# Optimization experiments

Measured on AMD Instinct MI355X. Metric: run time of the kernel, lower is better.

Reference implementation:

```python
import jax, jax.numpy as jnp
import numpy as np

# Architecture constants (from init_kwargs / Mamba2 defaults)
NL = 4          # num_layer per direction
DM = 256        # d_model (attention_in)
DS = 128        # d_state
DC = 4          # d_conv
DI = 2 * DM     # d_inner = expand * d_model = 512
HD = 64         # headdim
NH = DI // HD   # nheads = 8
NG = 1          # ngroups
D_XBC = DI + 2 * NG * DS           # 768 conv channels
D_INP = 2 * DI + 2 * NG * DS + NH  # 1288 in_proj width
EPS = 1e-5


def rmsnorm(x, w):
    return x * jax.lax.rsqrt(jnp.mean(x * x, axis=-1, keepdims=True) + EPS) * w


def causal_dwconv(x, w, b):
    # x: (B, L, C); w: (C, K); b: (C,) -- causal depthwise conv
    K = w.shape[1]
    L = x.shape[1]
    xp = jnp.pad(x, ((0, 0), (K - 1, 0), (0, 0)))
    y = b
    for k in range(K):  # K=4, fixed small kernel
        y = y + xp[:, k:k + L, :] * w[:, k]
    return y


def ssd_scan(xh, dt, A_log, Bm, Cm):
    # xh: (B,L,H,P), dt: (B,L,H), A_log: (H,), Bm/Cm: (B,L,N) (ngroups=1, broadcast over heads)
    A = -jnp.exp(A_log)                 # (H,)
    decay = jnp.exp(dt * A)             # (B,L,H)
    dtx = dt[..., None] * xh            # (B,L,H,P)
    B, L, H, P = xh.shape
    N = Bm.shape[-1]

    def step(h, inp):
        dec, u, bt, ct = inp            # (B,H), (B,H,P), (B,N), (B,N)
        h = h * dec[..., None, None] + u[..., None] * bt[:, None, None, :]
        y = jnp.einsum('bhpn,bn->bhp', h, ct)
        return h, y

    h0 = jnp.zeros((B, H, P, N), xh.dtype)
    xs = (jnp.moveaxis(decay, 1, 0), jnp.moveaxis(dtx, 1, 0),
          jnp.moveaxis(Bm, 1, 0), jnp.moveaxis(Cm, 1, 0))
    _, ys = jax.lax.scan(step, h0, xs)  # ys: (L,B,H,P)
    return jnp.moveaxis(ys, 0, 1)


def mamba2_mixer(u, Wi, cw, cb, dtb, Al, Dp, gw, Wo):
    B, L, _ = u.shape
    zxbcdt = u @ Wi                                   # (B,L,1288)
    z = zxbcdt[..., :DI]
    xBC = zxbcdt[..., DI:DI + D_XBC]
    dt = zxbcdt[..., DI + D_XBC:]
    xBC = jax.nn.silu(causal_dwconv(xBC, cw, cb))
    xh = xBC[..., :DI].reshape(B, L, NH, HD)
    Bm = xBC[..., DI:DI + NG * DS]
    Cm = xBC[..., DI + NG * DS:]
    dt = jax.nn.softplus(dt + dtb)                    # (B,L,H)
    y = ssd_scan(xh, dt, Al, Bm, Cm) + xh * Dp[None, None, :, None]
    y = y.reshape(B, L, DI)
    g = rmsnorm(y * jax.nn.silu(z), gw)               # RMSNormGated
    return g @ Wo


def run_stack(x, block_ids, nw, Wi, cw, cb, dtb, Al, Dp, gw, Wo):
    res = None
    h = x
    for i in block_ids:
        res = h + res if res is not None else h
        h = mamba2_mixer(rmsnorm(res, nw[i]), Wi[i], cw[i], cb[i],
                         dtb[i], Al[i], Dp[i], gw[i], Wo[i])
    return h + res


def setup_inputs() -> dict:
    key = jax.random.key(0)
    ks = jax.random.split(key, 8)
    B, L = 4, 2048
    NB = 2 * NL  # 8 blocks: forward + backward
    x = jax.random.normal(ks[0], (B, L, DM), jnp.float32)
    nw = jnp.ones((NB, DM), jnp.float32)
    Wi = jax.random.normal(ks[1], (NB, DM, D_INP), jnp.float32) * 0.02
    cw = jax.random.normal(ks[2], (NB, D_XBC, DC), jnp.float32) * 0.2
    cb = jnp.zeros((NB, D_XBC), jnp.float32)
    dt0 = jax.random.uniform(ks[3], (NB, NH), jnp.float32, 0.001, 0.1)
    dtb = dt0 + jnp.log(-jnp.expm1(-dt0))  # inverse softplus
    Al = jnp.log(jax.random.uniform(ks[4], (NB, NH), jnp.float32, 1.0, 16.0))
    Dp = jnp.ones((NB, NH), jnp.float32)
    gw = jnp.ones((NB, DI), jnp.float32)
    Wo = jax.random.normal(ks[5], (NB, DI, DM), jnp.float32) * 0.02
    return {"x": x, "block_norm_w": nw, "in_proj_w": Wi, "conv_w": cw,
            "conv_b": cb, "dt_bias": dtb, "A_log": Al, "D": Dp,
            "gnorm_w": gw, "out_proj_w": Wo}


def reference(x, block_norm_w, in_proj_w, conv_w, conv_b, dt_bias, A_log, D, gnorm_w, out_proj_w):
    fwd = run_stack(x, range(NL), block_norm_w, in_proj_w, conv_w, conv_b,
                    dt_bias, A_log, D, gnorm_w, out_proj_w)
    bwd = run_stack(jnp.flip(x, 1), range(NL, 2 * NL), block_norm_w, in_proj_w,
                    conv_w, conv_b, dt_bias, A_log, D, gnorm_w, out_proj_w)
    return fwd + jnp.flip(bwd, 1)  # bidirectional_merging='add'
```

## Files before the change

### kernel.cpp

```cpp
#include <hip/hip_runtime.h>
#include <hip/hip_bf16.h>
#include <math.h>

#define LSEQ 2048
#define BREAL 4
#define BT 8
#define DM 256
#define DI 512
#define DSZ 128
#define NHEADS 8
#define HDIM 64
#define DXBC 768
#define DINP 1288
#define NINP_PAD 1408
#define NLAYERS 4
#define QCH 64
#define NCH (LSEQ/QCH)
#define CTL 64
#define EPSF 1e-5f

typedef __attribute__((ext_vector_type(8))) short short8b;
typedef __attribute__((ext_vector_type(4))) float f32x4;

__device__ __forceinline__ float siluf(float x){ return x / (1.f + __expf(-x)); }
__device__ __forceinline__ unsigned short f2bf(float x){
    union { float f; unsigned u; } c; c.f = x;
    unsigned r = (c.u + 0x7FFFu + ((c.u >> 16) & 1u)) >> 16;
    return (unsigned short)r;
}
__device__ __forceinline__ float bf2f(unsigned short u){
    union { unsigned u; float f; } c; c.u = ((unsigned)u) << 16;
    return c.f;
}

__global__ __launch_bounds__(256) void k_prep(const float* __restrict__ x, float* __restrict__ res){
    int i = blockIdx.x*256 + threadIdx.x;
    int d4 = i & (DM/4 - 1);
    int t  = i >> 6;
    int l  = t % LSEQ;
    int b  = t / LSEQ;
    const float4* x4 = (const float4*)x;
    float4 v;
    if (b < BREAL) v = x4[((size_t)(b*LSEQ) + l)*(DM/4) + d4];
    else           v = x4[((size_t)((b-BREAL)*LSEQ) + (LSEQ-1-l))*(DM/4) + d4];
    ((float4*)res)[i] = v;
}

__global__ __launch_bounds__(256) void k_wtrans(const float* __restrict__ W, unsigned short* __restrict__ WT,
                                                int K, int N, int Npad){
    __shared__ float sT[32][33];
    int n0 = blockIdx.x*32, k0 = blockIdx.y*32, g = blockIdx.z;
    const float* Wg = W + (size_t)g*K*N;
    unsigned short* WTg = WT + (size_t)g*Npad*K;
    int t = threadIdx.x;
    int r = t >> 3, c4 = (t & 7)*4;
    float4 v;
    if (n0 + c4 + 3 < N) v = *(const float4*)(Wg + (size_t)(k0+r)*N + n0 + c4);
    else {
        float tmp[4];
        #pragma unroll
        for (int j = 0; j < 4; j++) tmp[j] = (n0 + c4 + j < N) ? Wg[(size_t)(k0+r)*N + n0 + c4 + j] : 0.f;
        v = make_float4(tmp[0],tmp[1],tmp[2],tmp[3]);
    }
    sT[c4+0][r] = v.x; sT[c4+1][r] = v.y; sT[c4+2][r] = v.z; sT[c4+3][r] = v.w;
    __syncthreads();
    ushort4 o;
    o.x = f2bf(sT[r][c4+0]); o.y = f2bf(sT[r][c4+1]); o.z = f2bf(sT[r][c4+2]); o.w = f2bf(sT[r][c4+3]);
    *(ushort4*)(WTg + (size_t)(n0+r)*K + k0 + c4) = o;
}

__global__ __launch_bounds__(256) void k_resnorm(float* __restrict__ res, const float* __restrict__ h,
                                                 const float* __restrict__ nw, int li, int addH,
                                                 unsigned short* __restrict__ u){
    int wid  = (blockIdx.x*256 + threadIdx.x) >> 6;
    int lane = threadIdx.x & 63;
    int b = wid / LSEQ;
    float* rr = res + (size_t)wid*DM;
    float4 v = ((float4*)rr)[lane];
    if (addH){
        float4 hv = ((const float4*)(h + (size_t)wid*DM))[lane];
        v.x += hv.x; v.y += hv.y; v.z += hv.z; v.w += hv.w;
        ((float4*)rr)[lane] = v;
    }
    float ss = v.x*v.x + v.y*v.y + v.z*v.z + v.w*v.w;
    #pragma unroll
    for (int o = 32; o >= 1; o >>= 1) ss += __shfl_xor(ss, o, 64);
    float sc = rsqrtf(ss*(1.f/DM) + EPSF);
    int blk = (b < BREAL) ? li : li + NLAYERS;
    float4 w = ((const float4*)(nw + (size_t)blk*DM))[lane];
    ushort4 o4;
    o4.x = f2bf(v.x*sc*w.x); o4.y = f2bf(v.y*sc*w.y); o4.z = f2bf(v.z*sc*w.z); o4.w = f2bf(v.w*sc*w.w);
    *(ushort4*)(u + (size_t)wid*DM + lane*4) = o4;
}

__global__ __launch_bounds__(256) void k_gemm_mfma(const unsigned short* __restrict__ A,
                                                   const unsigned short* __restrict__ WT,
                                                   int K, int N, size_t wt_group_stride, int rows_per_group,
                                                   float* __restrict__ Cf, unsigned short* __restrict__ Cb,
                                                   int write_bf16){
    __shared__ unsigned short sA[128][40];
    __shared__ unsigned short sW[128][40];
    int bn = blockIdx.x, bm = blockIdx.y;
    int row0 = bm*128, n0 = bn*128;
    const unsigned short* WTg = WT + (size_t)(row0 / rows_per_group) * wt_group_stride;
    int t = threadIdx.x;
    int w = t >> 6, lane = t & 63;
    int wr = w >> 1, wc = w & 1;
    int l15 = lane & 15, lg = lane >> 4;
    f32x4 acc[4][4];
    #pragma unroll
    for (int mi = 0; mi < 4; mi++)
        #pragma unroll
        for (int ni = 0; ni < 4; ni++) acc[mi][ni] = (f32x4){0.f,0.f,0.f,0.f};

    int srow = t >> 1, shalf = t & 1;
    const unsigned short* Ap = A + (size_t)(row0 + srow)*K + shalf*16;
    const unsigned short* Wp = WTg + (size_t)(n0 + srow)*K + shalf*16;

    for (int k0 = 0; k0 < K; k0 += 32){
        int4 a0 = *(const int4*)(Ap + k0);
        int4 a1 = *(const int4*)(Ap + k0 + 8);
        int4 w0 = *(const int4*)(Wp + k0);
        int4 w1 = *(const int4*)(Wp + k0 + 8);
        __syncthreads();
        *(int4*)&sA[srow][shalf*16]     = a0;
        *(int4*)&sA[srow][shalf*16 + 8] = a1;
        *(int4*)&sW[srow][shalf*16]     = w0;
        *(int4*)&sW[srow][shalf*16 + 8] = w1;
        __syncthreads();
        short8b af[4], bf[4];
        #pragma unroll
        for (int mi = 0; mi < 4; mi++) af[mi] = *(const short8b*)&sA[wr*64 + mi*16 + l15][lg*8];
        #pragma unroll
        for (int ni = 0; ni < 4; ni++) bf[ni] = *(const short8b*)&sW[wc*64 + ni*16 + l15][lg*8];
        #pragma unroll
        for (int mi = 0; mi < 4; mi++)
            #pragma unroll
            for (int ni = 0; ni < 4; ni++)
                acc[mi][ni] = __builtin_amdgcn_mfma_f32_16x16x32_bf16(af[mi], bf[ni], acc[mi][ni], 0, 0, 0);
    }
    if (write_bf16){
        #pragma unroll
        for (int mi = 0; mi < 4; mi++)
            #pragma unroll
            for (int ni = 0; ni < 4; ni++){
                int col = n0 + wc*64 + ni*16 + l15;
                if (col < N){
                    #pragma unroll
                    for (int r = 0; r < 4; r++){
                        int row = row0 + wr*64 + mi*16 + lg*4 + r;
                        Cb[(size_t)row*N + col] = f2bf(acc[mi][ni][r]);
                    }
                }
            }
    } else {
        #pragma unroll
        for (int mi = 0; mi < 4; mi++)
            #pragma unroll
            for (int ni = 0; ni < 4; ni++){
                int col = n0 + wc*64 + ni*16 + l15;
                if (col < N){
                    #pragma unroll
                    for (int r = 0; r < 4; r++){
                        int row = row0 + wr*64 + mi*16 + lg*4 + r;
                        Cf[(size_t)row*N + col] = acc[mi][ni][r];
                    }
                }
            }
    }
}

__global__ __launch_bounds__(256) void k_conv2(const unsigned short* __restrict__ zxb,
                                               const float* __restrict__ cw, const float* __restrict__ cb,
                                               int li, unsigned short* __restrict__ xbcb){
    int bid = blockIdx.x;
    int ch = bid % 3;
    int tl = (bid/3) % (LSEQ/CTL);
    int b  = bid / (3*(LSEQ/CTL));
    int c  = ch*256 + threadIdx.x;
    int blk = (b < BREAL) ? li : li + NLAYERS;
    float4 wv = *(const float4*)(cw + (size_t)blk*DXBC*4 + c*4);
    float bias = cb[(size_t)blk*DXBC + c];
    int l0 = tl*CTL;
    size_t base = ((size_t)b*LSEQ)*DINP + DI + c;
    float xm3 = (l0 >= 3) ? bf2f(zxb[base + (size_t)(l0-3)*DINP]) : 0.f;
    float xm2 = (l0 >= 2) ? bf2f(zxb[base + (size_t)(l0-2)*DINP]) : 0.f;
    float xm1 = (l0 >= 1) ? bf2f(zxb[base + (size_t)(l0-1)*DINP]) : 0.f;
    for (int l = l0; l < l0 + CTL; l++){
        float xv = bf2f(zxb[base + (size_t)l*DINP]);
        float acc = bias + xm3*wv.x + xm2*wv.y + xm1*wv.z + xv*wv.w;
        xbcb[((size_t)(b*LSEQ)+l)*DXBC + c] = f2bf(siluf(acc));
        xm3 = xm2; xm2 = xm1; xm1 = xv;
    }
}

__global__ __launch_bounds__(256) void k_dtla(const unsigned short* __restrict__ zxb,
                                              const float* __restrict__ dtb, const float* __restrict__ Al,
                                              int li, float* __restrict__ dt, float* __restrict__ la){
    int i = blockIdx.x*256 + threadIdx.x;
    int h = i & 7;
    int bl = i >> 3;
    int b = bl >> 11;
    int blk = (b < BREAL) ? li : li + NLAYERS;
    float raw = bf2f(zxb[(size_t)bl*DINP + DI + DXBC + h]) + dtb[blk*NHEADS + h];
    float d = (raw > 20.f) ? raw : log1pf(__expf(raw));
    float Aa = -__expf(Al[blk*NHEADS + h]);
    dt[i] = d;
    la[i] = d*Aa;
}

__global__ __launch_bounds__(256) void k_chunk_state(const unsigned short* __restrict__ xbcb,
                                                     const float* __restrict__ dt, const float* __restrict__ la,
                                                     unsigned short* __restrict__ states, float* __restrict__ decp){
    __shared__ unsigned short sBT[DSZ][72];
    __shared__ unsigned short sXT[HDIM][72];
    __shared__ float sSa[QCH];
    __shared__ float sW[QCH];
    int bid = blockIdx.x;
    int c  = bid & (NCH-1);
    int bh = bid >> 5;
    int b = bh >> 3, h = bh & 7;
    int t = threadIdx.x;
    size_t bl0 = (size_t)b*LSEQ + c*QCH;

    if (t < QCH){
        float v = la[(bl0 + t)*NHEADS + h];
        #pragma unroll
        for (int o = 1; o < 64; o <<= 1){
            float u = __shfl_up(v, o, 64);
            if (t >= o) v += u;
        }
        sSa[t] = v;
        float saQ = __shfl(v, 63, 64);
        float dtv = dt[(bl0 + t)*NHEADS + h];
        sW[t] = dtv * __expf(saQ - v);
        if (t == 63) decp[bh*NCH + c] = __expf(v);
    }
    __syncthreads();

    #pragma unroll
    for (int it = 0; it < 4; it++){
        int e = t + 256*it;
        int j = e >> 4, n8 = (e & 15)*8;
        int4 v = *(const int4*)(xbcb + (bl0 + j)*DXBC + DI + n8);
        const unsigned short* pv = (const unsigned short*)&v;
        #pragma unroll
        for (int i = 0; i < 8; i++) sBT[n8+i][j] = pv[i];
    }
    #pragma unroll
    for (int it = 0; it < 4; it++){
        int e = t + 256*it;
        int j = e >> 4, p4 = (e & 15)*4;
        ushort4 v = *(const ushort4*)(xbcb + (bl0 + j)*DXBC + h*HDIM + p4);
        float s = sW[j];
        sXT[p4+0][j] = f2bf(bf2f(v.x)*s);
        sXT[p4+1][j] = f2bf(bf2f(v.y)*s);
        sXT[p4+2][j] = f2bf(bf2f(v.z)*s);
        sXT[p4+3][j] = f2bf(bf2f(v.w)*s);
    }
    __syncthreads();

    int w = t >> 6, lane = t & 63, l15 = lane & 15, lg = lane >> 4;
    int p0 = (w >> 1)*32, n0 = (w & 1)*64;
    f32x4 acc[2][4];
    #pragma unroll
    for (int mi = 0; mi < 2; mi++)
        #pragma unroll
        for (int ni = 0; ni < 4; ni++) acc[mi][ni] = (f32x4){0.f,0.f,0.f,0.f};
    #pragma unroll
    for (int kk = 0; kk < 2; kk++){
        short8b a[2], bb[4];
        #pragma unroll
        for (int mi = 0; mi < 2; mi++) a[mi]  = *(const short8b*)&sXT[p0 + mi*16 + l15][kk*32 + lg*8];
        #pragma unroll
        for (int ni = 0; ni < 4; ni++) bb[ni] = *(const short8b*)&sBT[n0 + ni*16 + l15][kk*32 + lg*8];
        #pragma unroll
        for (int mi = 0; mi < 2; mi++)
            #pragma unroll
            for (int ni = 0; ni < 4; ni++)
                acc[mi][ni] = __builtin_amdgcn_mfma_f32_16x16x32_bf16(a[mi], bb[ni], acc[mi][ni], 0, 0, 0);
    }
    unsigned short* sp = states + ((size_t)bh*NCH + c)*(HDIM*DSZ);
    #pragma unroll
    for (int mi = 0; mi < 2; mi++)
        #pragma unroll
        for (int ni = 0; ni < 4; ni++)
            #pragma unroll
            for (int r = 0; r < 4; r++){
                int p = p0 + mi*16 + lg*4 + r;
                int n = n0 + ni*16 + l15;
                sp[(size_t)p*DSZ + n] = f2bf(acc[mi][ni][r]);
            }
}

__global__ __launch_bounds__(256) void k_scan2(unsigned short* __restrict__ states, const float* __restrict__ decp){
    int bh = blockIdx.x >> 3, slice = blockIdx.x & 7;
    int t = threadIdx.x;
    size_t base = (size_t)bh*NCH*(HDIM*DSZ) + slice*1024 + t*4;
    float H0=0.f, H1=0.f, H2=0.f, H3=0.f;
    for (int c = 0; c < NCH; c++){
        float P = decp[bh*NCH + c];
        unsigned short* sp = states + base + (size_t)c*(HDIM*DSZ);
        ushort4 S = *(ushort4*)sp;
        ushort4 Hw;
        Hw.x = f2bf(H0); Hw.y = f2bf(H1); Hw.z = f2bf(H2); Hw.w = f2bf(H3);
        *(ushort4*)sp = Hw;
        H0 = fmaf(H0, P, bf2f(S.x));
        H1 = fmaf(H1, P, bf2f(S.y));
        H2 = fmaf(H2, P, bf2f(S.z));
        H3 = fmaf(H3, P, bf2f(S.w));
    }
}

__global__ __launch_bounds__(256) void k_chunk_y(const unsigned short* __restrict__ xbcb,
                                                 const float* __restrict__ dt, const float* __restrict__ la,
                                                 const unsigned short* __restrict__ states,
                                                 const float* __restrict__ Dp, int li,
                                                 float* __restrict__ y){
    __shared__ unsigned short sC_[QCH][136];
    __shared__ unsigned short sB_[QCH][136];
    __shared__ unsigned short sH[HDIM][136];
    __shared__ unsigned short sS[QCH][72];
    __shared__ unsigned short sXT[HDIM][72];
    __shared__ float sSa[QCH];
    __shared__ float sDt[QCH];
    int bid = blockIdx.x;
    int c  = bid & (NCH-1);
    int bh = bid >> 5;
    int b = bh >> 3, h = bh & 7;
    int blk = (b < BREAL) ? li : li + NLAYERS;
    int t = threadIdx.x;
    size_t bl0 = (size_t)b*LSEQ + c*QCH;

    if (t < QCH){
        float v = la[(bl0 + t)*NHEADS + h];
        #pragma unroll
        for (int o = 1; o < 64; o <<= 1){
            float u = __shfl_up(v, o, 64);
            if (t >= o) v += u;
        }
        sSa[t] = v;
        sDt[t] = dt[(bl0 + t)*NHEADS + h];
    }
    __syncthreads();

    #pragma unroll
    for (int it = 0; it < 4; it++){
        int e = t + 256*it;
        int j = e >> 4, n8 = (e & 15)*8;
        *(int4*)&sB_[j][n8] = *(const int4*)(xbcb + (bl0 + j)*DXBC + DI + n8);
        *(int4*)&sC_[j][n8] = *(const int4*)(xbcb + (bl0 + j)*DXBC + DI + DSZ + n8);
    }
    {
        size_t sbase = ((size_t)bh*NCH + c)*(HDIM*DSZ);
        #pragma unroll
        for (int it = 0; it < 4; it++){
            int e = t + 256*it;
            int p = e >> 4, n8 = (e & 15)*8;
            *(int4*)&sH[p][n8] = *(const int4*)(states + sbase + (size_t)p*DSZ + n8);
        }
    }
    #pragma unroll
    for (int it = 0; it < 4; it++){
        int e = t + 256*it;
        int j = e >> 4, p4 = (e & 15)*4;
        ushort4 v = *(const ushort4*)(xbcb + (bl0 + j)*DXBC + h*HDIM + p4);
        float s = sDt[j];
        sXT[p4+0][j] = f2bf(bf2f(v.x)*s);
        sXT[p4+1][j] = f2bf(bf2f(v.y)*s);
        sXT[p4+2][j] = f2bf(bf2f(v.z)*s);
        sXT[p4+3][j] = f2bf(bf2f(v.w)*s);
    }
    __syncthreads();

    int w = t >> 6, lane = t & 63, l15 = lane & 15, lg = lane >> 4;
    int i0 = (w >> 1)*32, q0 = (w & 1)*32;

    f32x4 accS[2][2];
    #pragma unroll
    for (int mi = 0; mi < 2; mi++)
        #pragma unroll
        for (int nj = 0; nj < 2; nj++) accS[mi][nj] = (f32x4){0.f,0.f,0.f,0.f};
    #pragma unroll
    for (int kk = 0; kk < 4; kk++){
        short8b a[2], bb[2];
        #pragma unroll
        for (int mi = 0; mi < 2; mi++) a[mi]  = *(const short8b*)&sC_[i0 + mi*16 + l15][kk*32 + lg*8];
        #pragma unroll
        for (int nj = 0; nj < 2; nj++) bb[nj] = *(const short8b*)&sB_[q0 + nj*16 + l15][kk*32 + lg*8];
        #pragma unroll
        for (int mi = 0; mi < 2; mi++)
            #pragma unroll
            for (int nj = 0; nj < 2; nj++)
                accS[mi][nj] = __builtin_amdgcn_mfma_f32_16x16x32_bf16(a[mi], bb[nj], accS[mi][nj], 0, 0, 0);
    }
    #pragma unroll
    for (int mi = 0; mi < 2; mi++)
        #pragma unroll
        for (int nj = 0; nj < 2; nj++)
            #pragma unroll
            for (int r = 0; r < 4; r++){
                int i = i0 + mi*16 + lg*4 + r;
                int j = q0 + nj*16 + l15;
                float wgt = (i >= j) ? __expf(sSa[i] - sSa[j]) : 0.f;
                sS[i][j] = f2bf(accS[mi][nj][r] * wgt);
            }
    __syncthreads();

    f32x4 accY[2][2], accI[2][2];
    #pragma unroll
    for (int mi = 0; mi < 2; mi++)
        #pragma unroll
        for (int nj = 0; nj < 2; nj++){ accY[mi][nj] = (f32x4){0.f,0.f,0.f,0.f}; accI[mi][nj] = (f32x4){0.f,0.f,0.f,0.f}; }
    #pragma unroll
    for (int kk = 0; kk < 2; kk++){
        short8b a[2], bb[2];
        #pragma unroll
        for (int mi = 0; mi < 2; mi++) a[mi]  = *(const short8b*)&sS[i0 + mi*16 + l15][kk*32 + lg*8];
        #pragma unroll
        for (int nj = 0; nj < 2; nj++) bb[nj] = *(const short8b*)&sXT[q0 + nj*16 + l15][kk*32 + lg*8];
        #pragma unroll
        for (int mi = 0; mi < 2; mi++)
            #pragma unroll
            for (int nj = 0; nj < 2; nj++)
                accY[mi][nj] = __builtin_amdgcn_mfma_f32_16x16x32_bf16(a[mi], bb[nj], accY[mi][nj], 0, 0, 0);
    }
    #pragma unroll
    for (int kk = 0; kk < 4; kk++){
        short8b a[2], bb[2];
        #pragma unroll
        for (int mi = 0; mi < 2; mi++) a[mi]  = *(const short8b*)&sC_[i0 + mi*16 + l15][kk*32 + lg*8];
        #pragma unroll
        for (int nj = 0; nj < 2; nj++) bb[nj] = *(const short8b*)&sH[q0 + nj*16 + l15][kk*32 + lg*8];
        #pragma unroll
        for (int mi = 0; mi < 2; mi++)
            #pragma unroll
            for (int nj = 0; nj < 2; nj++)
                accI[mi][nj] = __builtin_amdgcn_mfma_f32_16x16x32_bf16(a[mi], bb[nj], accI[mi][nj], 0, 0, 0);
    }

    float dD = Dp[blk*NHEADS + h];
    #pragma unroll
    for (int mi = 0; mi < 2; mi++)
        #pragma unroll
        for (int r = 0; r < 4; r++){
            int i = i0 + mi*16 + lg*4 + r;
            float ei = __expf(sSa[i]);
            #pragma unroll
            for (int nj = 0; nj < 2; nj++){
                int p = q0 + nj*16 + l15;
                float xh = bf2f(xbcb[(bl0 + i)*DXBC + h*HDIM + p]);
                y[(bl0 + i)*DI + h*HDIM + p] = accY[mi][nj][r] + ei*accI[mi][nj][r] + dD*xh;
            }
        }
}

__global__ __launch_bounds__(256) void k_gatenorm(const float* __restrict__ y, const unsigned short* __restrict__ zxb,
                                                  const float* __restrict__ gw, int li,
                                                  unsigned short* __restrict__ yb){
    int wid  = (blockIdx.x*256 + threadIdx.x) >> 6;
    int lane = threadIdx.x & 63;
    int b = wid / LSEQ;
    int blk = (b < BREAL) ? li : li + NLAYERS;
    const float* yr = y + (size_t)wid*DI;
    const unsigned short* zr = zxb + (size_t)wid*DINP;
    float4 v0 = ((const float4*)yr)[lane];
    float4 v1 = ((const float4*)yr)[64 + lane];
    ushort4 zu0 = *(const ushort4*)(zr + lane*4);
    ushort4 zu1 = *(const ushort4*)(zr + 256 + lane*4);
    v0.x *= siluf(bf2f(zu0.x)); v0.y *= siluf(bf2f(zu0.y)); v0.z *= siluf(bf2f(zu0.z)); v0.w *= siluf(bf2f(zu0.w));
    v1.x *= siluf(bf2f(zu1.x)); v1.y *= siluf(bf2f(zu1.y)); v1.z *= siluf(bf2f(zu1.z)); v1.w *= siluf(bf2f(zu1.w));
    float ss = v0.x*v0.x + v0.y*v0.y + v0.z*v0.z + v0.w*v0.w
             + v1.x*v1.x + v1.y*v1.y + v1.z*v1.z + v1.w*v1.w;
    #pragma unroll
    for (int o = 32; o >= 1; o >>= 1) ss += __shfl_xor(ss, o, 64);
    float sc = rsqrtf(ss*(1.f/DI) + EPSF);
    const float4* w4 = (const float4*)(gw + (size_t)blk*DI);
    float4 w0 = w4[lane], w1 = w4[64 + lane];
    ushort4 o0, o1;
    o0.x = f2bf(v0.x*sc*w0.x); o0.y = f2bf(v0.y*sc*w0.y); o0.z = f2bf(v0.z*sc*w0.z); o0.w = f2bf(v0.w*sc*w0.w);
    o1.x = f2bf(v1.x*sc*w1.x); o1.y = f2bf(v1.y*sc*w1.y); o1.z = f2bf(v1.z*sc*w1.z); o1.w = f2bf(v1.w*sc*w1.w);
    *(ushort4*)(yb + (size_t)wid*DI + lane*4)       = o0;
    *(ushort4*)(yb + (size_t)wid*DI + 256 + lane*4) = o1;
}

__global__ __launch_bounds__(256) void k_final(const float* __restrict__ res, const float* __restrict__ h,
                                               float* __restrict__ out){
    int i = blockIdx.x*256 + threadIdx.x;
    int d4 = i & 63;
    int t  = i >> 6;
    int l = t % LSEQ, b = t / LSEQ;
    size_t fi = ((size_t)(b*LSEQ) + l)*(DM/4) + d4;
    size_t bi = ((size_t)((b+BREAL)*LSEQ) + (LSEQ-1-l))*(DM/4) + d4;
    float4 r1 = ((const float4*)res)[fi], h1 = ((const float4*)h)[fi];
    float4 r2 = ((const float4*)res)[bi], h2 = ((const float4*)h)[bi];
    float4 o;
    o.x = r1.x + h1.x + r2.x + h2.x;
    o.y = r1.y + h1.y + r2.y + h2.y;
    o.z = r1.z + h1.z + r2.z + h2.z;
    o.w = r1.w + h1.w + r2.w + h2.w;
    ((float4*)out)[i] = o;
}

extern "C" void kernel_launch(void* const* d_in, const int* in_sizes, int n_in,
                              void* d_out, int out_size, void* d_ws, size_t ws_size,
                              hipStream_t stream){
    const float* x   = (const float*)d_in[0];
    const float* nw  = (const float*)d_in[1];
    const float* Wi  = (const float*)d_in[2];
    const float* cw  = (const float*)d_in[3];
    const float* cb  = (const float*)d_in[4];
    const float* dtb = (const float*)d_in[5];
    const float* Al  = (const float*)d_in[6];
    const float* Dp  = (const float*)d_in[7];
    const float* gw  = (const float*)d_in[8];
    const float* Wo  = (const float*)d_in[9];
    float* out = (float*)d_out;

    size_t off = 0;
    auto alloc = [&](size_t bytes){ void* p = (char*)d_ws + off; off += (bytes + 255) & ~(size_t)255; return p; };
    float* RES    = (float*)alloc((size_t)BT*LSEQ*DM*4);
    unsigned short* STATES = (unsigned short*)alloc((size_t)BT*NHEADS*NCH*HDIM*DSZ*2);
    float* HBUF   = (float*)STATES;
    unsigned short* YGB = (unsigned short*)alloc((size_t)BT*LSEQ*DI*2);
    unsigned short* UBUF = YGB;
    unsigned short* ZXB = (unsigned short*)alloc((size_t)BT*LSEQ*DINP*2);
    unsigned short* XBC = (unsigned short*)alloc((size_t)BT*LSEQ*DXBC*2);
    float* DT     = (float*)alloc((size_t)BT*LSEQ*NHEADS*4);
    float* LA     = (float*)alloc((size_t)BT*LSEQ*NHEADS*4);
    float* YG     = (float*)alloc((size_t)BT*LSEQ*DI*4);
    float* DECP   = (float*)alloc((size_t)BT*NHEADS*NCH*4);
    unsigned short* WiT = (unsigned short*)alloc((size_t)2*NLAYERS*NINP_PAD*DM*2);
    unsigned short* WoT = (unsigned short*)alloc((size_t)2*NLAYERS*DM*DI*2);
    (void)ws_size; (void)in_sizes; (void)n_in; (void)out_size;

    k_prep<<<(BT*LSEQ*DM/4)/256, 256, 0, stream>>>(x, RES);
    k_wtrans<<<dim3(NINP_PAD/32, DM/32, 2*NLAYERS), 256, 0, stream>>>(Wi, WiT, DM, DINP, NINP_PAD);
    k_wtrans<<<dim3(DM/32, DI/32, 2*NLAYERS), 256, 0, stream>>>(Wo, WoT, DI, DM, DM);

    for (int li = 0; li < NLAYERS; li++){
        k_resnorm<<<(BT*LSEQ)/4, 256, 0, stream>>>(RES, HBUF, nw, li, li > 0 ? 1 : 0, UBUF);
        k_gemm_mfma<<<dim3(NINP_PAD/128, (BT*LSEQ)/128), 256, 0, stream>>>(
            UBUF, WiT + (size_t)li*NINP_PAD*DM, DM, DINP,
            (size_t)NLAYERS*NINP_PAD*DM, BREAL*LSEQ, nullptr, ZXB, 1);
        k_conv2<<<BT*(LSEQ/CTL)*3, 256, 0, stream>>>(ZXB, cw, cb, li, XBC);
        k_dtla<<<(BT*LSEQ*NHEADS)/256, 256, 0, stream>>>(ZXB, dtb, Al, li, DT, LA);
        k_chunk_state<<<BT*NHEADS*NCH, 256, 0, stream>>>(XBC, DT, LA, STATES, DECP);
        k_scan2<<<BT*NHEADS*8, 256, 0, stream>>>(STATES, DECP);
        k_chunk_y<<<BT*NHEADS*NCH, 256, 0, stream>>>(XBC, DT, LA, STATES, Dp, li, YG);
        k_gatenorm<<<(BT*LSEQ)/4, 256, 0, stream>>>(YG, ZXB, gw, li, YGB);
        k_gemm_mfma<<<dim3(DM/128, (BT*LSEQ)/128), 256, 0, stream>>>(
            YGB, WoT + (size_t)li*DM*DI, DI, DM,
            (size_t)NLAYERS*DM*DI, BREAL*LSEQ, HBUF, nullptr, 0);
    }
    k_final<<<(BREAL*LSEQ*DM/4)/256, 256, 0, stream>>>(RES, HBUF, out);
}
```

Before: 709.2 us.

## Fuse residual add into out_proj GEMM, merge dt kernel, batch heads per chunk block

The out_proj GEMM now accumulates straight into the residual buffer, which removes the separate H buffer and the residual add in resnorm and k_final. The dt/softplus computation is folded into the conv kernel, saving one launch. chunk_state and chunk_y each handle four heads per block so the B/C loads and the C·B^T product are shared across heads. The y intermediate is stored as bf16 instead of fp32, halving that traffic at some precision cost. Per-head loops add syncs and fewer blocks, which may reduce parallelism.

```diff
diff --git a/kernel.cpp b/kernel.cpp
--- a/kernel.cpp
+++ b/kernel.cpp
@@ -69,19 +69,14 @@
     *(ushort4*)(WTg + (size_t)(n0+r)*K + k0 + c4) = o;
 }
 
-__global__ __launch_bounds__(256) void k_resnorm(float* __restrict__ res, const float* __restrict__ h,
-                                                 const float* __restrict__ nw, int li, int addH,
+__global__ __launch_bounds__(256) void k_resnorm(const float* __restrict__ res,
+                                                 const float* __restrict__ nw, int li,
                                                  unsigned short* __restrict__ u){
     int wid  = (blockIdx.x*256 + threadIdx.x) >> 6;
     int lane = threadIdx.x & 63;
     int b = wid / LSEQ;
-    float* rr = res + (size_t)wid*DM;
-    float4 v = ((float4*)rr)[lane];
-    if (addH){
-        float4 hv = ((const float4*)(h + (size_t)wid*DM))[lane];
-        v.x += hv.x; v.y += hv.y; v.z += hv.z; v.w += hv.w;
-        ((float4*)rr)[lane] = v;
-    }
+    const float* rr = res + (size_t)wid*DM;
+    float4 v = ((const float4*)rr)[lane];
     float ss = v.x*v.x + v.y*v.y + v.z*v.z + v.w*v.w;
     #pragma unroll
     for (int o = 32; o >= 1; o >>= 1) ss += __shfl_xor(ss, o, 64);
@@ -97,7 +92,7 @@
                                                    const unsigned short* __restrict__ WT,
                                                    int K, int N, size_t wt_group_stride, int rows_per_group,
                                                    float* __restrict__ Cf, unsigned short* __restrict__ Cb,
-                                                   int write_bf16){
+                                                   int mode){
     __shared__ unsigned short sA[128][40];
     __shared__ unsigned short sW[128][40];
     int bn = blockIdx.x, bm = blockIdx.y;
@@ -139,40 +134,28 @@
             for (int ni = 0; ni < 4; ni++)
                 acc[mi][ni] = __builtin_amdgcn_mfma_f32_16x16x32_bf16(af[mi], bf[ni], acc[mi][ni], 0, 0, 0);
     }
-    if (write_bf16){
-        #pragma unroll
-        for (int mi = 0; mi < 4; mi++)
-            #pragma unroll
-            for (int ni = 0; ni < 4; ni++){
-                int col = n0 + wc*64 + ni*16 + l15;
-                if (col < N){
-                    #pragma unroll
-                    for (int r = 0; r < 4; r++){
-                        int row = row0 + wr*64 + mi*16 + lg*4 + r;
-                        Cb[(size_t)row*N + col] = f2bf(acc[mi][ni][r]);
-                    }
+    #pragma unroll
+    for (int mi = 0; mi < 4; mi++)
+        #pragma unroll
+        for (int ni = 0; ni < 4; ni++){
+            int col = n0 + wc*64 + ni*16 + l15;
+            if (col < N){
+                #pragma unroll
+                for (int r = 0; r < 4; r++){
+                    int row = row0 + wr*64 + mi*16 + lg*4 + r;
+                    if (mode == 1)      Cb[(size_t)row*N + col] = f2bf(acc[mi][ni][r]);
+                    else if (mode == 2) Cf[(size_t)row*N + col] += acc[mi][ni][r];
+                    else                Cf[(size_t)row*N + col] = acc[mi][ni][r];
                 }
             }
-    } else {
-        #pragma unroll
-        for (int mi = 0; mi < 4; mi++)
-            #pragma unroll
-            for (int ni = 0; ni < 4; ni++){
-                int col = n0 + wc*64 + ni*16 + l15;
-                if (col < N){
-                    #pragma unroll
-                    for (int r = 0; r < 4; r++){
-                        int row = row0 + wr*64 + mi*16 + lg*4 + r;
-                        Cf[(size_t)row*N + col] = acc[mi][ni][r];
-                    }
-                }
-            }
-    }
+        }
 }
 
 __global__ __launch_bounds__(256) void k_conv2(const unsigned short* __restrict__ zxb,
                                                const float* __restrict__ cw, const float* __restrict__ cb,
-                                               int li, unsigned short* __restrict__ xbcb){
+                                               const float* __restrict__ dtb, const float* __restrict__ Al,
+                                               int li, unsigned short* __restrict__ xbcb,
+                                               float* __restrict__ dtO, float* __restrict__ laO){
     int bid = blockIdx.x;
     int ch = bid % 3;
     int tl = (bid/3) % (LSEQ/CTL);
@@ -192,21 +175,18 @@
         xbcb[((size_t)(b*LSEQ)+l)*DXBC + c] = f2bf(siluf(acc));
         xm3 = xm2; xm2 = xm1; xm1 = xv;
     }
-}
-
-__global__ __launch_bounds__(256) void k_dtla(const unsigned short* __restrict__ zxb,
-                                              const float* __restrict__ dtb, const float* __restrict__ Al,
-                                              int li, float* __restrict__ dt, float* __restrict__ la){
-    int i = blockIdx.x*256 + threadIdx.x;
-    int h = i & 7;
-    int bl = i >> 3;
-    int b = bl >> 11;
-    int blk = (b < BREAL) ? li : li + NLAYERS;
-    float raw = bf2f(zxb[(size_t)bl*DINP + DI + DXBC + h]) + dtb[blk*NHEADS + h];
-    float d = (raw > 20.f) ? raw : log1pf(__expf(raw));
-    float Aa = -__expf(Al[blk*NHEADS + h]);
-    dt[i] = d;
-    la[i] = d*Aa;
+    if (ch == 0){
+        #pragma unroll
+        for (int it = 0; it < 2; it++){
+            int e = threadIdx.x*2 + it;
+            int h = e & 7, dl = e >> 3;
+            size_t bl = (size_t)b*LSEQ + l0 + dl;
+            float raw = bf2f(zxb[bl*DINP + DI + DXBC + h]) + dtb[blk*NHEADS + h];
+            float d = (raw > 20.f) ? raw : log1pf(__expf(raw));
+            dtO[bl*NHEADS + h] = d;
+            laO[bl*NHEADS + h] = -d*__expf(Al[blk*NHEADS + h]);
+        }
+    }
 }
 
 __global__ __launch_bounds__(256) void k_chunk_state(const unsigned short* __restrict__ xbcb,
@@ -214,30 +194,28 @@
                                                      unsigned short* __restrict__ states, float* __restrict__ decp){
     __shared__ unsigned short sBT[DSZ][72];
     __shared__ unsigned short sXT[HDIM][72];
-    __shared__ float sSa[QCH];
-    __shared__ float sW[QCH];
+    __shared__ float sW[4][QCH];
     int bid = blockIdx.x;
-    int c  = bid & (NCH-1);
-    int bh = bid >> 5;
-    int b = bh >> 3, h = bh & 7;
+    int hg = bid & 1;
+    int c  = (bid >> 1) & (NCH-1);
+    int b  = bid >> 6;
     int t = threadIdx.x;
+    int w = t >> 6, lane = t & 63, l15 = lane & 15, lg = lane >> 4;
     size_t bl0 = (size_t)b*LSEQ + c*QCH;
 
-    if (t < QCH){
-        float v = la[(bl0 + t)*NHEADS + h];
+    {
+        int h = hg*4 + w;
+        float v = la[(bl0 + lane)*NHEADS + h];
         #pragma unroll
         for (int o = 1; o < 64; o <<= 1){
             float u = __shfl_up(v, o, 64);
-            if (t >= o) v += u;
-        }
-        sSa[t] = v;
+            if (lane >= o) v += u;
+        }
         float saQ = __shfl(v, 63, 64);
-        float dtv = dt[(bl0 + t)*NHEADS + h];
-        sW[t] = dtv * __expf(saQ - v);
-        if (t == 63) decp[bh*NCH + c] = __expf(v);
-    }
-    __syncthreads();
-
+        float dtv = dt[(bl0 + lane)*NHEADS + h];
+        sW[w][lane] = dtv * __expf(saQ - v);
+        if (lane == 63) decp[((size_t)b*NHEADS + h)*NCH + c] = __expf(v);
+    }
     #pragma unroll
     for (int it = 0; it < 4; it++){
         int e = t + 256*it;
@@ -247,50 +225,54 @@
         #pragma unroll
         for (int i = 0; i < 8; i++) sBT[n8+i][j] = pv[i];
     }
-    #pragma unroll
-    for (int it = 0; it < 4; it++){
-        int e = t + 256*it;
-        int j = e >> 4, p4 = (e & 15)*4;
-        ushort4 v = *(const ushort4*)(xbcb + (bl0 + j)*DXBC + h*HDIM + p4);
-        float s = sW[j];
-        sXT[p4+0][j] = f2bf(bf2f(v.x)*s);
-        sXT[p4+1][j] = f2bf(bf2f(v.y)*s);
-        sXT[p4+2][j] = f2bf(bf2f(v.z)*s);
-        sXT[p4+3][j] = f2bf(bf2f(v.w)*s);
-    }
     __syncthreads();
 
-    int w = t >> 6, lane = t & 63, l15 = lane & 15, lg = lane >> 4;
     int p0 = (w >> 1)*32, n0 = (w & 1)*64;
-    f32x4 acc[2][4];
-    #pragma unroll
-    for (int mi = 0; mi < 2; mi++)
-        #pragma unroll
-        for (int ni = 0; ni < 4; ni++) acc[mi][ni] = (f32x4){0.f,0.f,0.f,0.f};
-    #pragma unroll
-    for (int kk = 0; kk < 2; kk++){
-        short8b a[2], bb[4];
-        #pragma unroll
-        for (int mi = 0; mi < 2; mi++) a[mi]  = *(const short8b*)&sXT[p0 + mi*16 + l15][kk*32 + lg*8];
-        #pragma unroll
-        for (int ni = 0; ni < 4; ni++) bb[ni] = *(const short8b*)&sBT[n0 + ni*16 + l15][kk*32 + lg*8];
+    for (int hh = 0; hh < 4; hh++){
+        int h = hg*4 + hh;
+        #pragma unroll
+        for (int it = 0; it < 4; it++){
+            int e = t + 256*it;
+            int j = e >> 4, p4 = (e & 15)*4;
+            ushort4 v = *(const ushort4*)(xbcb + (bl0 + j)*DXBC + h*HDIM + p4);
+            float s = sW[hh][j];
+            sXT[p4+0][j] = f2bf(bf2f(v.x)*s);
+            sXT[p4+1][j] = f2bf(bf2f(v.y)*s);
+            sXT[p4+2][j] = f2bf(bf2f(v.z)*s);
+            sXT[p4+3][j] = f2bf(bf2f(v.w)*s);
+        }
+        __syncthreads();
+        f32x4 acc[2][4];
         #pragma unroll
         for (int mi = 0; mi < 2; mi++)
             #pragma unroll
+            for (int ni = 0; ni < 4; ni++) acc[mi][ni] = (f32x4){0.f,0.f,0.f,0.f};
+        #pragma unroll
+        for (int kk = 0; kk < 2; kk++){
+            short8b a[2], bb[4];
+            #pragma unroll
+            for (int mi = 0; mi < 2; mi++) a[mi]  = *(const short8b*)&sXT[p0 + mi*16 + l15][kk*32 + lg*8];
+            #pragma unroll
+            for (int ni = 0; ni < 4; ni++) bb[ni] = *(const short8b*)&sBT[n0 + ni*16 + l15][kk*32 + lg*8];
+            #pragma unroll
+            for (int mi = 0; mi < 2; mi++)
+                #pragma unroll
+                for (int ni = 0; ni < 4; ni++)
+                    acc[mi][ni] = __builtin_amdgcn_mfma_f32_16x16x32_bf16(a[mi], bb[ni], acc[mi][ni], 0, 0, 0);
+        }
+        unsigned short* sp = states + (((size_t)b*NHEADS + h)*NCH + c)*(HDIM*DSZ);
+        #pragma unroll
+        for (int mi = 0; mi < 2; mi++)
+            #pragma unroll
             for (int ni = 0; ni < 4; ni++)
-                acc[mi][ni] = __builtin_amdgcn_mfma_f32_16x16x32_bf16(a[mi], bb[ni], acc[mi][ni], 0, 0, 0);
-    }
-    unsigned short* sp = states + ((size_t)bh*NCH + c)*(HDIM*DSZ);
-    #pragma unroll
-    for (int mi = 0; mi < 2; mi++)
-        #pragma unroll
-        for (int ni = 0; ni < 4; ni++)
-            #pragma unroll
-            for (int r = 0; r < 4; r++){
-                int p = p0 + mi*16 + lg*4 + r;
-                int n = n0 + ni*16 + l15;
-                sp[(size_t)p*DSZ + n] = f2bf(acc[mi][ni][r]);
-            }
+                #pragma unroll
+                for (int r = 0; r < 4; r++){
+                    int p = p0 + mi*16 + lg*4 + r;
+                    int n = n0 + ni*16 + l15;
+                    sp[(size_t)p*DSZ + n] = f2bf(acc[mi][ni][r]);
+                }
+        __syncthreads();
+    }
 }
 
 __global__ __launch_bounds__(256) void k_scan2(unsigned short* __restrict__ states, const float* __restrict__ decp){
@@ -316,34 +298,34 @@
                                                  const float* __restrict__ dt, const float* __restrict__ la,
                                                  const unsigned short* __restrict__ states,
                                                  const float* __restrict__ Dp, int li,
-                                                 float* __restrict__ y){
+                                                 unsigned short* __restrict__ y){
+    __shared__ unsigned short sB_[QCH][136];
     __shared__ unsigned short sC_[QCH][136];
-    __shared__ unsigned short sB_[QCH][136];
-    __shared__ unsigned short sH[HDIM][136];
     __shared__ unsigned short sS[QCH][72];
     __shared__ unsigned short sXT[HDIM][72];
-    __shared__ float sSa[QCH];
-    __shared__ float sDt[QCH];
+    __shared__ unsigned short sH[HDIM][136];
+    __shared__ float sSa[4][QCH];
+    __shared__ float sDt[4][QCH];
     int bid = blockIdx.x;
-    int c  = bid & (NCH-1);
-    int bh = bid >> 5;
-    int b = bh >> 3, h = bh & 7;
+    int hg = bid & 1;
+    int c  = (bid >> 1) & (NCH-1);
+    int b  = bid >> 6;
     int blk = (b < BREAL) ? li : li + NLAYERS;
     int t = threadIdx.x;
+    int w = t >> 6, lane = t & 63, l15 = lane & 15, lg = lane >> 4;
     size_t bl0 = (size_t)b*LSEQ + c*QCH;
 
-    if (t < QCH){
-        float v = la[(bl0 + t)*NHEADS + h];
+    {
+        int h = hg*4 + w;
+        float v = la[(bl0 + lane)*NHEADS + h];
         #pragma unroll
         for (int o = 1; o < 64; o <<= 1){
             float u = __shfl_up(v, o, 64);
-            if (t >= o) v += u;
-        }
-        sSa[t] = v;
-        sDt[t] = dt[(bl0 + t)*NHEADS + h];
-    }
-    __syncthreads();
-
+            if (lane >= o) v += u;
+        }
+        sSa[w][lane] = v;
+        sDt[w][lane] = dt[(bl0 + lane)*NHEADS + h];
+    }
     #pragma unroll
     for (int it = 0; it < 4; it++){
         int e = t + 256*it;
@@ -351,125 +333,132 @@
         *(int4*)&sB_[j][n8] = *(const int4*)(xbcb + (bl0 + j)*DXBC + DI + n8);
         *(int4*)&sC_[j][n8] = *(const int4*)(xbcb + (bl0 + j)*DXBC + DI + DSZ + n8);
     }
-    {
-        size_t sbase = ((size_t)bh*NCH + c)*(HDIM*DSZ);
+    __syncthreads();
+
+    int i0 = (w >> 1)*32, q0 = (w & 1)*32;
+
+    f32x4 accS[2][2];
+    #pragma unroll
+    for (int mi = 0; mi < 2; mi++)
+        #pragma unroll
+        for (int nj = 0; nj < 2; nj++) accS[mi][nj] = (f32x4){0.f,0.f,0.f,0.f};
+    #pragma unroll
+    for (int kk = 0; kk < 4; kk++){
+        short8b a[2], bb[2];
+        #pragma unroll
+        for (int mi = 0; mi < 2; mi++) a[mi]  = *(const short8b*)&sC_[i0 + mi*16 + l15][kk*32 + lg*8];
+        #pragma unroll
+        for (int nj = 0; nj < 2; nj++) bb[nj] = *(const short8b*)&sB_[q0 + nj*16 + l15][kk*32 + lg*8];
+        #pragma unroll
+        for (int mi = 0; mi < 2; mi++)
+            #pragma unroll
+            for (int nj = 0; nj < 2; nj++)
+                accS[mi][nj] = __builtin_amdgcn_mfma_f32_16x16x32_bf16(a[mi], bb[nj], accS[mi][nj], 0, 0, 0);
+    }
+
+    for (int hh = 0; hh < 4; hh++){
+        int h = hg*4 + hh;
+        #pragma unroll
+        for (int mi = 0; mi < 2; mi++)
+            #pragma unroll
+            for (int nj = 0; nj < 2; nj++)
+                #pragma unroll
+                for (int r = 0; r < 4; r++){
+                    int i = i0 + mi*16 + lg*4 + r;
+                    int j = q0 + nj*16 + l15;
+                    float wgt = (i >= j) ? __expf(sSa[hh][i] - sSa[hh][j]) : 0.f;
+                    sS[i][j] = f2bf(accS[mi][nj][r] * wgt);
+                }
         #pragma unroll
         for (int it = 0; it < 4; it++){
             int e = t + 256*it;
-            int p = e >> 4, n8 = (e & 15)*8;
-            *(int4*)&sH[p][n8] = *(const int4*)(states + sbase + (size_t)p*DSZ + n8);
-        }
-    }
-    #pragma unroll
-    for (int it = 0; it < 4; it++){
-        int e = t + 256*it;
-        int j = e >> 4, p4 = (e & 15)*4;
-        ushort4 v = *(const ushort4*)(xbcb + (bl0 + j)*DXBC + h*HDIM + p4);
-        float s = sDt[j];
-        sXT[p4+0][j] = f2bf(bf2f(v.x)*s);
-        sXT[p4+1][j] = f2bf(bf2f(v.y)*s);
-        sXT[p4+2][j] = f2bf(bf2f(v.z)*s);
-        sXT[p4+3][j] = f2bf(bf2f(v.w)*s);
-    }
-    __syncthreads();
-
-    int w = t >> 6, lane = t & 63, l15 = lane & 15, lg = lane >> 4;
-    int i0 = (w >> 1)*32, q0 = (w & 1)*32;
-
-    f32x4 accS[2][2];
-    #pragma unroll
-    for (int mi = 0; mi < 2; mi++)
-        #pragma unroll
-        for (int nj = 0; nj < 2; nj++) accS[mi][nj] = (f32x4){0.f,0.f,0.f,0.f};
-    #pragma unroll
-    for (int kk = 0; kk < 4; kk++){
-        short8b a[2], bb[2];
-        #pragma unroll
-        for (int mi = 0; mi < 2; mi++) a[mi]  = *(const short8b*)&sC_[i0 + mi*16 + l15][kk*32 + lg*8];
-        #pragma unroll
-        for (int nj = 0; nj < 2; nj++) bb[nj] = *(const short8b*)&sB_[q0 + nj*16 + l15][kk*32 + lg*8];
+            int j = e >> 4, p4 = (e & 15)*4;
+            ushort4 v = *(const ushort4*)(xbcb + (bl0 + j)*DXBC + h*HDIM + p4);
+            float s = sDt[hh][j];
+            sXT[p4+0][j] = f2bf(bf2f(v.x)*s);
+            sXT[p4+1][j] = f2bf(bf2f(v.y)*s);
+            sXT[p4+2][j] = f2bf(bf2f(v.z)*s);
+            sXT[p4+3][j] = f2bf(bf2f(v.w)*s);
+        }
+        {
+            size_t sbase = (((size_t)b*NHEADS + h)*NCH + c)*(HDIM*DSZ);
+            #pragma unroll
+            for (int it = 0; it < 4; it++){
+                int e = t + 256*it;
+                int p = e >> 4, n8 = (e & 15)*8;
+                *(int4*)&sH[p][n8] = *(const int4*)(states + sbase + (size_t)p*DSZ + n8);
+            }
+        }
+        __syncthreads();
+
+        f32x4 accY[2][2], accI[2][2];
         #pragma unroll
         for (int mi = 0; mi < 2; mi++)
             #pragma unroll
-            for (int nj = 0; nj < 2; nj++)
-                accS[mi][nj] = __builtin_amdgcn_mfma_f32_16x16x32_bf16(a[mi], bb[nj], accS[mi][nj], 0, 0, 0);
-    }
-    #pragma unroll
-    for (int mi = 0; mi < 2; mi++)
-        #pragma unroll
-        for (int nj = 0; nj < 2; nj++)
+            for (int nj = 0; nj < 2; nj++){ accY[mi][nj] = (f32x4){0.f,0.f,0.f,0.f}; accI[mi][nj] = (f32x4){0.f,0.f,0.f,0.f}; }
+        #pragma unroll
+        for (int kk = 0; kk < 2; kk++){
+            short8b a[2], bb[2];
+            #pragma unroll
+            for (int mi = 0; mi < 2; mi++) a[mi]  = *(const short8b*)&sS[i0 + mi*16 + l15][kk*32 + lg*8];
+            #pragma unroll
+            for (int nj = 0; nj < 2; nj++) bb[nj] = *(const short8b*)&sXT[q0 + nj*16 + l15][kk*32 + lg*8];
+            #pragma unroll
+            for (int mi = 0; mi < 2; mi++)
+                #pragma unroll
+                for (int nj = 0; nj < 2; nj++)
+                    accY[mi][nj] = __builtin_amdgcn_mfma_f32_16x16x32_bf16(a[mi], bb[nj], accY[mi][nj], 0, 0, 0);
+        }
+        #pragma unroll
+        for (int kk = 0; kk < 4; kk++){
+            short8b a[2], bb[2];
+            #pragma unroll
+            for (int mi = 0; mi < 2; mi++) a[mi]  = *(const short8b*)&sC_[i0 + mi*16 + l15][kk*32 + lg*8];
+            #pragma unroll
+            for (int nj = 0; nj < 2; nj++) bb[nj] = *(const short8b*)&sH[q0 + nj*16 + l15][kk*32 + lg*8];
+            #pragma unroll
+            for (int mi = 0; mi < 2; mi++)
+                #pragma unroll
+                for (int nj = 0; nj < 2; nj++)
+                    accI[mi][nj] = __builtin_amdgcn_mfma_f32_16x16x32_bf16(a[mi], bb[nj], accI[mi][nj], 0, 0, 0);
+        }
+
+        float dD = Dp[blk*NHEADS + h];
+        #pragma unroll
+        for (int mi = 0; mi < 2; mi++)
             #pragma unroll
             for (int r = 0; r < 4; r++){
                 int i = i0 + mi*16 + lg*4 + r;
-                int j = q0 + nj*16 + l15;
-                float wgt = (i >= j) ? __expf(sSa[i] - sSa[j]) : 0.f;
-                sS[i][j] = f2bf(accS[mi][nj][r] * wgt);
+                float ei = __expf(sSa[hh][i]);
+                #pragma unroll
+                for (int nj = 0; nj < 2; nj++){
+                    int p = q0 + nj*16 + l15;
+                    float xh = bf2f(xbcb[(bl0 + i)*DXBC + h*HDIM + p]);
+                    y[(bl0 + i)*DI + h*HDIM + p] = f2bf(accY[mi][nj][r] + ei*accI[mi][nj][r] + dD*xh);
+                }
             }
-    __syncthreads();
-
-    f32x4 accY[2][2], accI[2][2];
-    #pragma unroll
-    for (int mi = 0; mi < 2; mi++)
-        #pragma unroll
-        for (int nj = 0; nj < 2; nj++){ accY[mi][nj] = (f32x4){0.f,0.f,0.f,0.f}; accI[mi][nj] = (f32x4){0.f,0.f,0.f,0.f}; }
-    #pragma unroll
-    for (int kk = 0; kk < 2; kk++){
-        short8b a[2], bb[2];
-        #pragma unroll
-        for (int mi = 0; mi < 2; mi++) a[mi]  = *(const short8b*)&sS[i0 + mi*16 + l15][kk*32 + lg*8];
-        #pragma unroll
-        for (int nj = 0; nj < 2; nj++) bb[nj] = *(const short8b*)&sXT[q0 + nj*16 + l15][kk*32 + lg*8];
-        #pragma unroll
-        for (int mi = 0; mi < 2; mi++)
-            #pragma unroll
-            for (int nj = 0; nj < 2; nj++)
-                accY[mi][nj] = __builtin_amdgcn_mfma_f32_16x16x32_bf16(a[mi], bb[nj], accY[mi][nj], 0, 0, 0);
-    }
-    #pragma unroll
-    for (int kk = 0; kk < 4; kk++){
-        short8b a[2], bb[2];
-        #pragma unroll
-        for (int mi = 0; mi < 2; mi++) a[mi]  = *(const short8b*)&sC_[i0 + mi*16 + l15][kk*32 + lg*8];
-        #pragma unroll
-        for (int nj = 0; nj < 2; nj++) bb[nj] = *(const short8b*)&sH[q0 + nj*16 + l15][kk*32 + lg*8];
-        #pragma unroll
-        for (int mi = 0; mi < 2; mi++)
-            #pragma unroll
-            for (int nj = 0; nj < 2; nj++)
-                accI[mi][nj] = __builtin_amdgcn_mfma_f32_16x16x32_bf16(a[mi], bb[nj], accI[mi][nj], 0, 0, 0);
-    }
-
-    float dD = Dp[blk*NHEADS + h];
-    #pragma unroll
-    for (int mi = 0; mi < 2; mi++)
-        #pragma unroll
-        for (int r = 0; r < 4; r++){
-            int i = i0 + mi*16 + lg*4 + r;
-            float ei = __expf(sSa[i]);
-            #pragma unroll
-            for (int nj = 0; nj < 2; nj++){
-                int p = q0 + nj*16 + l15;
-                float xh = bf2f(xbcb[(bl0 + i)*DXBC + h*HDIM + p]);
-                y[(bl0 + i)*DI + h*HDIM + p] = accY[mi][nj][r] + ei*accI[mi][nj][r] + dD*xh;
-            }
-        }
-}
-
-__global__ __launch_bounds__(256) void k_gatenorm(const float* __restrict__ y, const unsigned short* __restrict__ zxb,
+        __syncthreads();
+    }
+}
+
+__global__ __launch_bounds__(256) void k_gatenorm(const unsigned short* __restrict__ y, const unsigned short* __restrict__ zxb,
                                                   const float* __restrict__ gw, int li,
                                                   unsigned short* __restrict__ yb){
     int wid  = (blockIdx.x*256 + threadIdx.x) >> 6;
     int lane = threadIdx.x & 63;
     int b = wid / LSEQ;
     int blk = (b < BREAL) ? li : li + NLAYERS;
-    const float* yr = y + (size_t)wid*DI;
+    const unsigned short* yr = y + (size_t)wid*DI;
     const unsigned short* zr = zxb + (size_t)wid*DINP;
-    float4 v0 = ((const float4*)yr)[lane];
-    float4 v1 = ((const float4*)yr)[64 + lane];
+    ushort4 yu0 = *(const ushort4*)(yr + lane*4);
+    ushort4 yu1 = *(const ushort4*)(yr + 256 + lane*4);
     ushort4 zu0 = *(const ushort4*)(zr + lane*4);
     ushort4 zu1 = *(const ushort4*)(zr + 256 + lane*4);
-    v0.x *= siluf(bf2f(zu0.x)); v0.y *= siluf(bf2f(zu0.y)); v0.z *= siluf(bf2f(zu0.z)); v0.w *= siluf(bf2f(zu0.w));
-    v1.x *= siluf(bf2f(zu1.x)); v1.y *= siluf(bf2f(zu1.y)); v1.z *= siluf(bf2f(zu1.z)); v1.w *= siluf(bf2f(zu1.w));
+    float4 v0, v1;
+    v0.x = bf2f(yu0.x)*siluf(bf2f(zu0.x)); v0.y = bf2f(yu0.y)*siluf(bf2f(zu0.y));
+    v0.z = bf2f(yu0.z)*siluf(bf2f(zu0.z)); v0.w = bf2f(yu0.w)*siluf(bf2f(zu0.w));
+    v1.x = bf2f(yu1.x)*siluf(bf2f(zu1.x)); v1.y = bf2f(yu1.y)*siluf(bf2f(zu1.y));
+    v1.z = bf2f(yu1.z)*siluf(bf2f(zu1.z)); v1.w = bf2f(yu1.w)*siluf(bf2f(zu1.w));
     float ss = v0.x*v0.x + v0.y*v0.y + v0.z*v0.z + v0.w*v0.w
              + v1.x*v1.x + v1.y*v1.y + v1.z*v1.z + v1.w*v1.w;
     #pragma unroll
@@ -484,21 +473,20 @@
     *(ushort4*)(yb + (size_t)wid*DI + 256 + lane*4) = o1;
 }
 
-__global__ __launch_bounds__(256) void k_final(const float* __restrict__ res, const float* __restrict__ h,
-                                               float* __restrict__ out){
+__global__ __launch_bounds__(256) void k_final(const float* __restrict__ res, float* __restrict__ out){
     int i = blockIdx.x*256 + threadIdx.x;
     int d4 = i & 63;
     int t  = i >> 6;
     int l = t % LSEQ, b = t / LSEQ;
     size_t fi = ((size_t)(b*LSEQ) + l)*(DM/4) + d4;
     size_t bi = ((size_t)((b+BREAL)*LSEQ) + (LSEQ-1-l))*(DM/4) + d4;
-    float4 r1 = ((const float4*)res)[fi], h1 = ((const float4*)h)[fi];
-    float4 r2 = ((const float4*)res)[bi], h2 = ((const float4*)h)[bi];
+    float4 r1 = ((const float4*)res)[fi];
+    float4 r2 = ((const float4*)res)[bi];
     float4 o;
-    o.x = r1.x + h1.x + r2.x + h2.x;
-    o.y = r1.y + h1.y + r2.y + h2.y;
-    o.z = r1.z + h1.z + r2.z + h2.z;
-    o.w = r1.w + h1.w + r2.w + h2.w;
+    o.x = r1.x + r2.x;
+    o.y = r1.y + r2.y;
+    o.z = r1.z + r2.z;
+    o.w = r1.w + r2.w;
     ((float4*)out)[i] = o;
 }
 
@@ -521,14 +509,13 @@
     auto alloc = [&](size_t bytes){ void* p = (char*)d_ws + off; off += (bytes + 255) & ~(size_t)255; return p; };
     float* RES    = (float*)alloc((size_t)BT*LSEQ*DM*4);
     unsigned short* STATES = (unsigned short*)alloc((size_t)BT*NHEADS*NCH*HDIM*DSZ*2);
-    float* HBUF   = (float*)STATES;
     unsigned short* YGB = (unsigned short*)alloc((size_t)BT*LSEQ*DI*2);
     unsigned short* UBUF = YGB;
     unsigned short* ZXB = (unsigned short*)alloc((size_t)BT*LSEQ*DINP*2);
     unsigned short* XBC = (unsigned short*)alloc((size_t)BT*LSEQ*DXBC*2);
     float* DT     = (float*)alloc((size_t)BT*LSEQ*NHEADS*4);
     float* LA     = (float*)alloc((size_t)BT*LSEQ*NHEADS*4);
-    float* YG     = (float*)alloc((size_t)BT*LSEQ*DI*4);
+    unsigned short* YG = (unsigned short*)alloc((size_t)BT*LSEQ*DI*2);
     float* DECP   = (float*)alloc((size_t)BT*NHEADS*NCH*4);
     unsigned short* WiT = (unsigned short*)alloc((size_t)2*NLAYERS*NINP_PAD*DM*2);
     unsigned short* WoT = (unsigned short*)alloc((size_t)2*NLAYERS*DM*DI*2);
@@ -539,19 +526,18 @@
     k_wtrans<<<dim3(DM/32, DI/32, 2*NLAYERS), 256, 0, stream>>>(Wo, WoT, DI, DM, DM);
 
     for (int li = 0; li < NLAYERS; li++){
-        k_resnorm<<<(BT*LSEQ)/4, 256, 0, stream>>>(RES, HBUF, nw, li, li > 0 ? 1 : 0, UBUF);
+        k_resnorm<<<(BT*LSEQ)/4, 256, 0, stream>>>(RES, nw, li, UBUF);
         k_gemm_mfma<<<dim3(NINP_PAD/128, (BT*LSEQ)/128), 256, 0, stream>>>(
             UBUF, WiT + (size_t)li*NINP_PAD*DM, DM, DINP,
             (size_t)NLAYERS*NINP_PAD*DM, BREAL*LSEQ, nullptr, ZXB, 1);
-        k_conv2<<<BT*(LSEQ/CTL)*3, 256, 0, stream>>>(ZXB, cw, cb, li, XBC);
-        k_dtla<<<(BT*LSEQ*NHEADS)/256, 256, 0, stream>>>(ZXB, dtb, Al, li, DT, LA);
-        k_chunk_state<<<BT*NHEADS*NCH, 256, 0, stream>>>(XBC, DT, LA, STATES, DECP);
+        k_conv2<<<BT*(LSEQ/CTL)*3, 256, 0, stream>>>(ZXB, cw, cb, dtb, Al, li, XBC, DT, LA);
+        k_chunk_state<<<BT*NCH*2, 256, 0, stream>>>(XBC, DT, LA, STATES, DECP);
         k_scan2<<<BT*NHEADS*8, 256, 0, stream>>>(STATES, DECP);
-        k_chunk_y<<<BT*NHEADS*NCH, 256, 0, stream>>>(XBC, DT, LA, STATES, Dp, li, YG);
+        k_chunk_y<<<BT*NCH*2, 256, 0, stream>>>(XBC, DT, LA, STATES, Dp, li, YG);
         k_gatenorm<<<(BT*LSEQ)/4, 256, 0, stream>>>(YG, ZXB, gw, li, YGB);
         k_gemm_mfma<<<dim3(DM/128, (BT*LSEQ)/128), 256, 0, stream>>>(
             YGB, WoT + (size_t)li*DM*DI, DI, DM,
-            (size_t)NLAYERS*DM*DI, BREAL*LSEQ, HBUF, nullptr, 0);
-    }
-    k_final<<<(BREAL*LSEQ*DM/4)/256, 256, 0, stream>>>(RES, HBUF, out);
-}
+            (size_t)NLAYERS*DM*DI, BREAL*LSEQ, RES, nullptr, 2);
+    }
+    k_final<<<(BREAL*LSEQ*DM/4)/256, 256, 0, stream>>>(RES, out);
+}
```

After: 704.0 us. Within noise of the previous version (-0.7%).
